# Kernel tuning notes

Measured on AMD Instinct MI355X. Metric: run time of the kernel, lower is better.

## Reference

```python
import jax, jax.numpy as jnp
import numpy as np

H = 8
D_MODEL = 512
D_K = D_MODEL // H
NEG = -1e9


def setup_inputs() -> dict:
    key = jax.random.key(0)
    ks = jax.random.split(key, 12)
    N, Lq, Lk = 2, 4096, 4096
    inp = {
        "query": jax.random.normal(ks[0], (N, Lq, D_MODEL), dtype=jnp.float32),
        "key": jax.random.normal(ks[1], (N, Lk, D_MODEL), dtype=jnp.float32),
        "value": jax.random.normal(ks[2], (N, Lk, D_MODEL), dtype=jnp.float32),
        "mask": jnp.ones((N, 1, Lk), dtype=jnp.int32),
    }
    scale = 0.02
    for i, nm in enumerate(["q", "k", "v", "o"]):
        inp[f"W{nm}"] = scale * jax.random.normal(ks[3 + i], (D_MODEL, D_MODEL), dtype=jnp.float32)
        inp[f"b{nm}"] = jnp.zeros((D_MODEL,), dtype=jnp.float32)
    return inp


def reference(query, key, value, mask, Wq, bq, Wk, bk, Wv, bv, Wo, bo):
    # torch Linear: y = x @ W.T + b
    N, Lq, _ = query.shape
    Lk = key.shape[1]
    q = (query @ Wq.T + bq).reshape(N, Lq, H, D_K)   # (N,Lq,h,dk)
    k = (key @ Wk.T + bk).reshape(N, Lk, H, D_K)     # (N,Lk,h,dk)
    v = (value @ Wv.T + bv).reshape(N, Lk, H, D_K)   # (N,Lk,h,dk)
    # scores: (N,h,Lq,Lk)
    scores = jnp.einsum("bqhd,bkhd->bhqk", q, k) / jnp.sqrt(jnp.float32(D_K))
    # mask (N,1,Lk) or (N,Lq,Lk) -> broadcast over heads (and Lq if singleton)
    m = mask[:, None, :, :]  # (N,1,1|Lq,Lk)
    scores = jnp.where(m == 0, jnp.float32(NEG), scores)
    attn = jax.nn.softmax(scores, axis=-1)
    # dropout is identity in eval mode (deterministic reference)
    out = jnp.einsum("bhqk,bkhd->bqhd", attn, v).reshape(N, Lq, D_MODEL)
    return out @ Wo.T + bo
```

## Files before the change

kernel.cpp:

```cpp
#include <hip/hip_runtime.h>
#include <hip/hip_bf16.h>

#define H 8
#define DM 512
#define DK 64
#define LSEQ 4096
#define NB 2
#define NSPLIT 4
#define KSPAN (LSEQ / NSPLIT)
#define NIT (KSPAN / 64)

#define QSCALE 0.18033688011112042f

typedef float f32x4 __attribute__((ext_vector_type(4)));
typedef __bf16 bf16x8 __attribute__((ext_vector_type(8)));
typedef __bf16 bf16x2 __attribute__((ext_vector_type(2)));
typedef unsigned short u16;

__device__ __forceinline__ u16 f2bf(float f) {
    union { float f; unsigned u; } v{f};
    return (u16)((v.u + 0x8000u) >> 16);
}

__device__ __forceinline__ unsigned pkbf(float a, float b) {
#if __has_builtin(__builtin_amdgcn_cvt_pk_bf16_f32)
    union { bf16x2 v; unsigned u; } x;
    x.v = __builtin_amdgcn_cvt_pk_bf16_f32(a, b);
    return x.u;
#else
    union { float f; unsigned u; } x{a}, y{b};
    return ((x.u + 0x8000u) >> 16) | ((y.u + 0x8000u) & 0xffff0000u);
#endif
}

__device__ __forceinline__ ushort4 cvt4(float4 a) {
    union { ushort4 s; uint2 u; } o;
    o.u.x = pkbf(a.x, a.y);
    o.u.y = pkbf(a.z, a.w);
    return o.s;
}

__device__ __forceinline__ float2 ubf2(unsigned u) {
    union { float f; unsigned v; } a, b;
    a.v = u << 16;
    b.v = u & 0xffff0000u;
    return make_float2(a.f, b.f);
}

__device__ __forceinline__ float fexp2(float x) {
#if __has_builtin(__builtin_amdgcn_exp2f)
    return __builtin_amdgcn_exp2f(x);
#else
    return exp2f(x);
#endif
}

__device__ __forceinline__ f32x4 mfma32(bf16x8 a, bf16x8 b, f32x4 c) {
    return __builtin_amdgcn_mfma_f32_16x16x32_bf16(a, b, c, 0, 0, 0);
}

__launch_bounds__(256, 8)
__global__ void cvt_all(const float* __restrict__ W0, const float* __restrict__ W1,
                        const float* __restrict__ W2, const float* __restrict__ W3,
                        const float* __restrict__ X0, const float* __restrict__ X1,
                        const float* __restrict__ X2,
                        u16* __restrict__ wout, u16* __restrict__ xout)
{
    const int y = blockIdx.y;
    const float* src;
    u16* dst;
    int nblk;
    if (y < 4) {
        src = (y == 0) ? W0 : (y == 1) ? W1 : (y == 2) ? W2 : W3;
        dst = wout + (size_t)y * DM * DM;
        nblk = (DM * DM) / (256 * 8);
    } else {
        src = (y == 4) ? X0 : (y == 5) ? X1 : X2;
        dst = xout + (size_t)(y - 4) * ((size_t)NB * LSEQ * DM);
        nblk = ((size_t)NB * LSEQ * DM) / (256 * 8);
    }
    if ((int)blockIdx.x >= nblk) return;
    size_t base = ((size_t)blockIdx.x * 256 + threadIdx.x) * 8;
    float4 a = *(const float4*)(src + base);
    float4 b = *(const float4*)(src + base + 4);
    *(ushort4*)(dst + base)     = cvt4(a);
    *(ushort4*)(dst + base + 4) = cvt4(b);
}

__launch_bounds__(256, 2)
__global__ void proj_qkv(const u16* __restrict__ xbf,
                         const u16* __restrict__ wbf,
                         const float* __restrict__ bq, const float* __restrict__ bk,
                         const float* __restrict__ bv,
                         const int* __restrict__ mask,
                         u16* __restrict__ qo, u16* __restrict__ ko, u16* __restrict__ vo)
{
    const int mode = blockIdx.z;
    const u16* X      = xbf + (size_t)mode * ((size_t)NB * LSEQ * DM);
    const u16* Wb     = wbf + (size_t)mode * DM * DM;
    const float* bias = (mode == 0) ? bq : (mode == 1) ? bk : bv;
    u16* out          = (mode == 0) ? qo : (mode == 1) ? ko : vo;

    __shared__ __align__(16) u16 As[2][128][72];
    __shared__ __align__(16) u16 Bs[2][128][72];

    const int tid  = threadIdx.x;
    const int wave = tid >> 6;
    const int lane = tid & 63;
    const int g    = lane >> 4;
    const int ln   = lane & 15;
    const int wr   = wave >> 1;
    const int wc   = wave & 1;

    const int m0 = blockIdx.x * 128;
    const int n0 = blockIdx.y * 128;

    uint4 xa[4], wa[4];
    #pragma unroll
    for (int i = 0; i < 4; ++i) {
        int idx = tid + 256 * i;
        int row = idx >> 3;
        int col = (idx & 7) * 8;
        xa[i] = *(const uint4*)(X  + (size_t)(m0 + row) * DM + col);
        wa[i] = *(const uint4*)(Wb + (size_t)(n0 + row) * DM + col);
    }
    #pragma unroll
    for (int i = 0; i < 4; ++i) {
        int idx = tid + 256 * i;
        int row = idx >> 3;
        int col = (idx & 7) * 8;
        *(uint4*)&As[0][row][col] = xa[i];
        *(uint4*)&Bs[0][row][col] = wa[i];
    }

    f32x4 acc[4][4] = {};

    for (int kt = 0; kt < 8; ++kt) {
        const int cur = kt & 1;
        __syncthreads();

        if (kt < 7) {
            int kb = (kt + 1) * 64;
            #pragma unroll
            for (int i = 0; i < 4; ++i) {
                int idx = tid + 256 * i;
                int row = idx >> 3;
                int col = (idx & 7) * 8;
                xa[i] = *(const uint4*)(X  + (size_t)(m0 + row) * DM + kb + col);
                wa[i] = *(const uint4*)(Wb + (size_t)(n0 + row) * DM + kb + col);
            }
        }

        bf16x8 af[4][2], bf[4][2];
        #pragma unroll
        for (int t = 0; t < 4; ++t) {
            af[t][0] = *(const bf16x8*)&As[cur][wr * 64 + t * 16 + ln][g * 8];
            af[t][1] = *(const bf16x8*)&As[cur][wr * 64 + t * 16 + ln][32 + g * 8];
            bf[t][0] = *(const bf16x8*)&Bs[cur][wc * 64 + t * 16 + ln][g * 8];
            bf[t][1] = *(const bf16x8*)&Bs[cur][wc * 64 + t * 16 + ln][32 + g * 8];
        }
        #pragma unroll
        for (int mt = 0; mt < 4; ++mt)
            #pragma unroll
            for (int nt = 0; nt < 4; ++nt) {
                acc[mt][nt] = mfma32(af[mt][0], bf[nt][0], acc[mt][nt]);
                acc[mt][nt] = mfma32(af[mt][1], bf[nt][1], acc[mt][nt]);
            }

        if (kt < 7) {
            int nxt = 1 - cur;
            #pragma unroll
            for (int i = 0; i < 4; ++i) {
                int idx = tid + 256 * i;
                int row = idx >> 3;
                int col = (idx & 7) * 8;
                *(uint4*)&As[nxt][row][col] = xa[i];
                *(uint4*)&Bs[nxt][row][col] = wa[i];
            }
        }
    }

    if (mode != 2) {
        #pragma unroll
        for (int nt = 0; nt < 4; ++nt) {
            int n  = n0 + wc * 64 + nt * 16 + ln;
            float bias_n = bias[n];
            int hh = n >> 6;
            int d  = n & (DK - 1);
            #pragma unroll
            for (int mt = 0; mt < 4; ++mt)
                #pragma unroll
                for (int r = 0; r < 4; ++r) {
                    int m  = m0 + wr * 64 + mt * 16 + g * 4 + r;
                    int bb = m >> 12;
                    int s  = m & (LSEQ - 1);
                    float val = acc[mt][nt][r] + bias_n;
                    if (mode == 0) val *= QSCALE;
                    else           val = mask[bb * LSEQ + s] ? val : 0.0f;
                    out[(size_t)((bb * H + hh) * LSEQ + s) * DK + d] = f2bf(val);
                }
        }
    } else {
        __syncthreads();
        u16* Ts = &As[0][0][0];
        const int bb = m0 >> 12;
        const int s0 = m0 & (LSEQ - 1);
        #pragma unroll
        for (int nt = 0; nt < 4; ++nt) {
            int dl = wc * 64 + nt * 16 + ln;
            float bias_n = bias[n0 + dl];
            #pragma unroll
            for (int mt = 0; mt < 4; ++mt)
                #pragma unroll
                for (int r = 0; r < 4; ++r) {
                    int sl = wr * 64 + mt * 16 + g * 4 + r;
                    float val = acc[mt][nt][r] + bias_n;
                    val = mask[bb * LSEQ + s0 + sl] ? val : 0.0f;
                    Ts[dl * 136 + sl] = f2bf(val);
                }
        }
        __syncthreads();
        int dl   = tid >> 1;
        int half = tid & 1;
        int n  = n0 + dl;
        int hh = n >> 6;
        int d  = n & (DK - 1);
        int sb = s0 + half * 64;
        u16* dst = out + ((size_t)((bb * H + hh) * DK + d) * LSEQ + sb);
        const u16* srcp = Ts + dl * 136 + half * 64;
        #pragma unroll
        for (int i = 0; i < 8; ++i)
            *(uint4*)(dst + i * 8) = *(const uint4*)(srcp + i * 8);
    }
}

__launch_bounds__(256, 4)
__global__ void flash(const u16* __restrict__ qws, const u16* __restrict__ kws,
                      const u16* __restrict__ vws, const int* __restrict__ mask,
                      u16* __restrict__ Opart, float* __restrict__ lpart)
{
    __shared__ u16 Ks[2][64][64];
    __shared__ u16 Vs[2][64][64];

    const int tid   = threadIdx.x;
    const int wave  = tid >> 6;
    const int lane  = tid & 63;
    const int g     = lane >> 4;
    const int ln    = lane & 15;
    const int b     = blockIdx.z;
    const int h     = blockIdx.y;
    const int qblk  = blockIdx.x & 31;
    const int split = blockIdx.x >> 5;
    const int q0    = qblk * 128;
    const int kstart = split * KSPAN;

    const u16* qp = qws + ((size_t)((b * H + h) * LSEQ) + q0 + wave * 32 + ln) * DK;
    const u16* kp = kws + (size_t)(b * H + h) * LSEQ * DK;
    const u16* vp = vws + (size_t)(b * H + h) * DK * LSEQ;
    const int* mp = mask + b * LSEQ;

    int nmask = 0;
    for (int t = 0; t < NIT; ++t) {
        int mval = mp[kstart + t * 64 + lane];
        unsigned long long bal = __ballot(mval == 0);
        nmask += (int)__popcll(bal);
    }
    const float fnmask = (float)nmask;

    bf16x8 qf[2][2];
    qf[0][0] = *(const bf16x8*)(qp + g * 8);
    qf[0][1] = *(const bf16x8*)(qp + 32 + g * 8);
    qf[1][0] = *(const bf16x8*)(qp + 16 * DK + g * 8);
    qf[1][1] = *(const bf16x8*)(qp + 16 * DK + 32 + g * 8);

    union OU { unsigned u[4]; bf16x8 v; } onesu;
    onesu.u[0] = onesu.u[1] = onesu.u[2] = onesu.u[3] = 0x3F803F80u;
    const bf16x8 vones = onesu.v;

    f32x4 accO[2][4] = {};
    f32x4 accL[2] = {};
    const f32x4 fzero = {};

    const int row = tid >> 3;
    const int c   = tid & 7;
    const int swz = row & 7;
    const int kcol = (c ^ swz) * 8;
    const int vcol0 = ((2 * c) & 3) * 16 + (c >> 1) * 4;
    const int vs0 = vcol0 >> 3;
    const int vof = vcol0 & 7;
    const int vw0 = ((vs0 ^ swz) * 8) + vof;
    const int vw1 = (((vs0 + 2) ^ swz) * 8) + vof;
    const int rs = ln & 7;

    uint4 kr0, kr1, vr0, vr1;
    kr0 = *(const uint4*)(kp + (size_t)(kstart + row) * DK + c * 8);
    kr1 = *(const uint4*)(kp + (size_t)(kstart + row + 32) * DK + c * 8);
    vr0 = *(const uint4*)(vp + (size_t)row * LSEQ + kstart + c * 8);
    vr1 = *(const uint4*)(vp + (size_t)(row + 32) * LSEQ + kstart + c * 8);
    *(uint4*)&Ks[0][row][kcol]      = kr0;
    *(uint4*)&Ks[0][row + 32][kcol] = kr1;
    *(uint2*)&Vs[0][row][vw0]       = make_uint2(vr0.x, vr0.y);
    *(uint2*)&Vs[0][row][vw1]       = make_uint2(vr0.z, vr0.w);
    *(uint2*)&Vs[0][row + 32][vw0]  = make_uint2(vr1.x, vr1.y);
    *(uint2*)&Vs[0][row + 32][vw1]  = make_uint2(vr1.z, vr1.w);

    for (int it = 0; it < NIT; ++it) {
        const int cur = it & 1;
        __syncthreads();

        if (it < NIT - 1) {
            int kn = kstart + it * 64 + 64;
            kr0 = *(const uint4*)(kp + (size_t)(kn + row) * DK + c * 8);
            kr1 = *(const uint4*)(kp + (size_t)(kn + row + 32) * DK + c * 8);
            vr0 = *(const uint4*)(vp + (size_t)row * LSEQ + kn + c * 8);
            vr1 = *(const uint4*)(vp + (size_t)(row + 32) * LSEQ + kn + c * 8);
        }

        __builtin_amdgcn_s_setprio(1);
        f32x4 sc[2][4];
        #pragma unroll
        for (int kb = 0; kb < 4; ++kb) {
            bf16x8 kf0 = *(const bf16x8*)&Ks[cur][kb * 16 + ln][(g ^ rs) * 8];
            bf16x8 kf1 = *(const bf16x8*)&Ks[cur][kb * 16 + ln][((g + 4) ^ rs) * 8];
            #pragma unroll
            for (int j = 0; j < 2; ++j) {
                f32x4 z = mfma32(kf0, qf[j][0], fzero);
                z = mfma32(kf1, qf[j][1], z);
                sc[j][kb] = z;
            }
        }
        __builtin_amdgcn_s_setprio(0);

        #pragma unroll
        for (int kb = 0; kb < 4; ++kb)
            #pragma unroll
            for (int j = 0; j < 2; ++j) {
                sc[j][kb][0] = fexp2(sc[j][kb][0]);
                sc[j][kb][1] = fexp2(sc[j][kb][1]);
                sc[j][kb][2] = fexp2(sc[j][kb][2]);
                sc[j][kb][3] = fexp2(sc[j][kb][3]);
            }

        union PU { unsigned u[4]; bf16x8 v; } p01[2], p23[2];
        #pragma unroll
        for (int j = 0; j < 2; ++j) {
            p01[j].u[0] = pkbf(sc[j][0][0], sc[j][0][1]);
            p01[j].u[1] = pkbf(sc[j][0][2], sc[j][0][3]);
            p01[j].u[2] = pkbf(sc[j][1][0], sc[j][1][1]);
            p01[j].u[3] = pkbf(sc[j][1][2], sc[j][1][3]);
            p23[j].u[0] = pkbf(sc[j][2][0], sc[j][2][1]);
            p23[j].u[1] = pkbf(sc[j][2][2], sc[j][2][3]);
            p23[j].u[2] = pkbf(sc[j][3][0], sc[j][3][1]);
            p23[j].u[3] = pkbf(sc[j][3][2], sc[j][3][3]);
        }

        __builtin_amdgcn_s_setprio(1);
        #pragma unroll
        for (int j = 0; j < 2; ++j) {
            accL[j] = mfma32(p01[j].v, vones, accL[j]);
            accL[j] = mfma32(p23[j].v, vones, accL[j]);
        }
        #pragma unroll
        for (int t = 0; t < 4; ++t) {
            bf16x8 vb01 = *(const bf16x8*)&Vs[cur][t * 16 + ln][((2 * g) ^ rs) * 8];
            bf16x8 vb23 = *(const bf16x8*)&Vs[cur][t * 16 + ln][((2 * g + 1) ^ rs) * 8];
            #pragma unroll
            for (int j = 0; j < 2; ++j) {
                accO[j][t] = mfma32(p01[j].v, vb01, accO[j][t]);
                accO[j][t] = mfma32(p23[j].v, vb23, accO[j][t]);
            }
        }
        __builtin_amdgcn_s_setprio(0);

        if (it < NIT - 1) {
            int nxt = 1 - cur;
            *(uint4*)&Ks[nxt][row][kcol]      = kr0;
            *(uint4*)&Ks[nxt][row + 32][kcol] = kr1;
            *(uint2*)&Vs[nxt][row][vw0]       = make_uint2(vr0.x, vr0.y);
            *(uint2*)&Vs[nxt][row][vw1]       = make_uint2(vr0.z, vr0.w);
            *(uint2*)&Vs[nxt][row + 32][vw0]  = make_uint2(vr1.x, vr1.y);
            *(uint2*)&Vs[nxt][row + 32][vw1]  = make_uint2(vr1.z, vr1.w);
        }
    }

    const size_t PLANE = (size_t)NB * LSEQ * DM;
    u16* opp = Opart + (size_t)split * PLANE;

    #pragma unroll
    for (int j = 0; j < 2; ++j) {
        if (ln == 0) {
            #pragma unroll
            for (int r = 0; r < 4; ++r)
                lpart[(size_t)split * (NB * H * LSEQ) + ((size_t)(b * H + h) * LSEQ)
                      + q0 + wave * 32 + j * 16 + g * 4 + r] = accL[j][r] - fnmask;
        }
        #pragma unroll
        for (int r = 0; r < 4; ++r) {
            float linv = 1.0f / (accL[j][r] - fnmask);
            size_t base = ((size_t)(b * LSEQ) + q0 + wave * 32 + j * 16 + g * 4 + r) * DM + h * DK;
            #pragma unroll
            for (int t = 0; t < 4; ++t)
                opp[base + t * 16 + ln] = f2bf(accO[j][t][r] * linv);
        }
    }
}

__launch_bounds__(256, 4)
__global__ void reduce_split(const u16* __restrict__ Opart, const float* __restrict__ lpart,
                             u16* __restrict__ ows)
{
    const size_t PLANE = (size_t)NB * LSEQ * DM;
    const size_t LP    = (size_t)NB * H * LSEQ;
    size_t gid  = (size_t)blockIdx.x * 256 + threadIdx.x;
    size_t flat = gid * 8;

    int b   = (int)(flat >> 21);
    int rem = (int)(flat & ((1 << 21) - 1));
    int q   = rem >> 9;
    int hh  = (rem & 511) >> 6;
    size_t lidx = ((size_t)(b * H + hh) * LSEQ) + q;

    float ls[NSPLIT];
    float lsum = 0.0f;
    #pragma unroll
    for (int s = 0; s < NSPLIT; ++s) {
        ls[s] = lpart[(size_t)s * LP + lidx];
        lsum += ls[s];
    }
    float inv = 1.0f / lsum;

    float o[8] = {};
    #pragma unroll
    for (int s = 0; s < NSPLIT; ++s) {
        float w = ls[s] * inv;
        uint4 cc = *(const uint4*)(Opart + (size_t)s * PLANE + flat);
        float2 a;
        a = ubf2(cc.x); o[0] += w * a.x; o[1] += w * a.y;
        a = ubf2(cc.y); o[2] += w * a.x; o[3] += w * a.y;
        a = ubf2(cc.z); o[4] += w * a.x; o[5] += w * a.y;
        a = ubf2(cc.w); o[6] += w * a.x; o[7] += w * a.y;
    }
    uint4 r;
    r.x = pkbf(o[0], o[1]);
    r.y = pkbf(o[2], o[3]);
    r.z = pkbf(o[4], o[5]);
    r.w = pkbf(o[6], o[7]);
    *(uint4*)(ows + flat) = r;
}

__launch_bounds__(256, 3)
__global__ void proj_out(const u16* __restrict__ A, const u16* __restrict__ Wob,
                         const float* __restrict__ bo, float* __restrict__ out)
{
    __shared__ __align__(16) u16 As[2][128][68];
    __shared__ __align__(16) u16 Bs[2][64][68];

    const int tid  = threadIdx.x;
    const int wave = tid >> 6;
    const int lane = tid & 63;
    const int g    = lane >> 4;
    const int ln   = lane & 15;

    const int m0 = blockIdx.x * 128;
    const int n0 = blockIdx.y * 64;

    uint4 aa[4];
    uint4 wbb[2];
    #pragma unroll
    for (int i = 0; i < 4; ++i) {
        int idx = tid + 256 * i;
        int row = idx >> 3;
        int col = (idx & 7) * 8;
        aa[i] = *(const uint4*)(A + (size_t)(m0 + row) * DM + col);
    }
    #pragma unroll
    for (int i = 0; i < 2; ++i) {
        int idx = tid + 256 * i;
        int rwb = idx >> 3;
        int cwb = (idx & 7) * 8;
        wbb[i] = *(const uint4*)(Wob + (size_t)(n0 + rwb) * DM + cwb);
    }
    #pragma unroll
    for (int i = 0; i < 4; ++i) {
        int idx = tid + 256 * i;
        int row = idx >> 3;
        int col = (idx & 7) * 8;
        *(uint4*)&As[0][row][col] = aa[i];
    }
    #pragma unroll
    for (int i = 0; i < 2; ++i) {
        int idx = tid + 256 * i;
        int rwb = idx >> 3;
        int cwb = (idx & 7) * 8;
        *(uint4*)&Bs[0][rwb][cwb] = wbb[i];
    }

    f32x4 acc[2][4] = {};

    for (int kt = 0; kt < 8; ++kt) {
        const int cur = kt & 1;
        __syncthreads();

        if (kt < 7) {
            int kb = (kt + 1) * 64;
            #pragma unroll
            for (int i = 0; i < 4; ++i) {
                int idx = tid + 256 * i;
                int row = idx >> 3;
                int col = (idx & 7) * 8;
                aa[i] = *(const uint4*)(A + (size_t)(m0 + row) * DM + kb + col);
            }
            #pragma unroll
            for (int i = 0; i < 2; ++i) {
                int idx = tid + 256 * i;
                int rwb = idx >> 3;
                int cwb = (idx & 7) * 8;
                wbb[i] = *(const uint4*)(Wob + (size_t)(n0 + rwb) * DM + kb + cwb);
            }
        }

        bf16x8 af[2][2], bf[4][2];
        #pragma unroll
        for (int mt = 0; mt < 2; ++mt) {
            af[mt][0] = *(const bf16x8*)&As[cur][wave * 32 + mt * 16 + ln][g * 8];
            af[mt][1] = *(const bf16x8*)&As[cur][wave * 32 + mt * 16 + ln][32 + g * 8];
        }
        #pragma unroll
        for (int nt = 0; nt < 4; ++nt) {
            bf[nt][0] = *(const bf16x8*)&Bs[cur][nt * 16 + ln][g * 8];
            bf[nt][1] = *(const bf16x8*)&Bs[cur][nt * 16 + ln][32 + g * 8];
        }
        #pragma unroll
        for (int mt = 0; mt < 2; ++mt)
            #pragma unroll
            for (int nt = 0; nt < 4; ++nt) {
                acc[mt][nt] = mfma32(af[mt][0], bf[nt][0], acc[mt][nt]);
                acc[mt][nt] = mfma32(af[mt][1], bf[nt][1], acc[mt][nt]);
            }

        if (kt < 7) {
            int nxt = 1 - cur;
            #pragma unroll
            for (int i = 0; i < 4; ++i) {
                int idx = tid + 256 * i;
                int row = idx >> 3;
                int col = (idx & 7) * 8;
                *(uint4*)&As[nxt][row][col] = aa[i];
            }
            #pragma unroll
            for (int i = 0; i < 2; ++i) {
                int idx = tid + 256 * i;
                int rwb = idx >> 3;
                int cwb = (idx & 7) * 8;
                *(uint4*)&Bs[nxt][rwb][cwb] = wbb[i];
            }
        }
    }

    #pragma unroll
    for (int nt = 0; nt < 4; ++nt) {
        int n = n0 + nt * 16 + ln;
        float bias_n = bo[n];
        #pragma unroll
        for (int mt = 0; mt < 2; ++mt)
            #pragma unroll
            for (int r = 0; r < 4; ++r) {
                int m = m0 + wave * 32 + mt * 16 + g * 4 + r;
                out[(size_t)m * DM + n] = acc[mt][nt][r] + bias_n;
            }
    }
}

extern "C" void kernel_launch(void* const* d_in, const int* in_sizes, int n_in,
                              void* d_out, int out_size, void* d_ws, size_t ws_size,
                              hipStream_t stream) {
    (void)in_sizes; (void)n_in; (void)out_size; (void)ws_size;

    const float* query = (const float*)d_in[0];
    const float* key   = (const float*)d_in[1];
    const float* value = (const float*)d_in[2];
    const int*   mask  = (const int*)d_in[3];
    const float* Wq = (const float*)d_in[4];
    const float* bq = (const float*)d_in[5];
    const float* Wk = (const float*)d_in[6];
    const float* bk = (const float*)d_in[7];
    const float* Wv = (const float*)d_in[8];
    const float* bv = (const float*)d_in[9];
    const float* Wo = (const float*)d_in[10];
    const float* bo = (const float*)d_in[11];
    float* out = (float*)d_out;

    const size_t PLANE = (size_t)NB * H * LSEQ * DK;
    u16* qws   = (u16*)d_ws;
    u16* kws   = qws + PLANE;
    u16* vws   = kws + PLANE;
    u16* ows   = vws + PLANE;
    u16* Opart = ows + PLANE;
    float* lpart = (float*)(Opart + (size_t)NSPLIT * PLANE);
    u16* wbf   = (u16*)(lpart + (size_t)NSPLIT * NB * H * LSEQ);
    u16* xbf   = Opart;

    dim3 blk(256);
    cvt_all<<<dim3(2048, 7), blk, 0, stream>>>(Wq, Wk, Wv, Wo, query, key, value,
                                               wbf, xbf);
    proj_qkv<<<dim3(64, 4, 3), blk, 0, stream>>>(xbf, wbf, bq, bk, bv, mask,
                                                 qws, kws, vws);
    flash<<<dim3(32 * NSPLIT, H, NB), blk, 0, stream>>>(qws, kws, vws, mask, Opart, lpart);
    reduce_split<<<dim3(2048), blk, 0, stream>>>(Opart, lpart, ows);
    proj_out<<<dim3(64, 8, 1), blk, 0, stream>>>(ows, wbf + 3 * (size_t)DM * DM, bo, out);
}
```

Before: 230.9 us.

## Fuse split-K reduction into flash kernel via last-block atomic counter

Removes the separate reduce_split launch. Each flash block increments a per-(batch, head, q-block) counter, and the last of the NSPLIT blocks to finish combines the partial outputs using the lpart weights and writes ows. The counters are zeroed by an extra grid row added to the conversion kernel. This saves one kernel launch and its pass over global memory, and lets the reduction overlap with flash blocks still running, at the cost of atomics, thread fences and a tail of extra work in some blocks.

```diff
diff --git a/kernel.cpp b/kernel.cpp
--- a/kernel.cpp
+++ b/kernel.cpp
@@ -64,9 +64,17 @@
                         const float* __restrict__ W2, const float* __restrict__ W3,
                         const float* __restrict__ X0, const float* __restrict__ X1,
                         const float* __restrict__ X2,
-                        u16* __restrict__ wout, u16* __restrict__ xout)
+                        u16* __restrict__ wout, u16* __restrict__ xout,
+                        int* __restrict__ cnt)
 {
     const int y = blockIdx.y;
+    if (y == 7) {
+        if (blockIdx.x == 0) {
+            cnt[threadIdx.x] = 0;
+            cnt[threadIdx.x + 256] = 0;
+        }
+        return;
+    }
     const float* src;
     u16* dst;
     int nblk;
@@ -237,7 +245,8 @@
 __launch_bounds__(256, 4)
 __global__ void flash(const u16* __restrict__ qws, const u16* __restrict__ kws,
                       const u16* __restrict__ vws, const int* __restrict__ mask,
-                      u16* __restrict__ Opart, float* __restrict__ lpart)
+                      u16* __restrict__ Opart, float* __restrict__ lpart,
+                      u16* __restrict__ ows, int* __restrict__ cnt)
 {
     __shared__ u16 Ks[2][64][64];
     __shared__ u16 Vs[2][64][64];
@@ -403,49 +412,62 @@
                 opp[base + t * 16 + ln] = f2bf(accO[j][t][r] * linv);
         }
     }
-}
-
-__launch_bounds__(256, 4)
-__global__ void reduce_split(const u16* __restrict__ Opart, const float* __restrict__ lpart,
-                             u16* __restrict__ ows)
-{
-    const size_t PLANE = (size_t)NB * LSEQ * DM;
-    const size_t LP    = (size_t)NB * H * LSEQ;
-    size_t gid  = (size_t)blockIdx.x * 256 + threadIdx.x;
-    size_t flat = gid * 8;
-
-    int b   = (int)(flat >> 21);
-    int rem = (int)(flat & ((1 << 21) - 1));
-    int q   = rem >> 9;
-    int hh  = (rem & 511) >> 6;
-    size_t lidx = ((size_t)(b * H + hh) * LSEQ) + q;
-
-    float ls[NSPLIT];
-    float lsum = 0.0f;
-    #pragma unroll
-    for (int s = 0; s < NSPLIT; ++s) {
-        ls[s] = lpart[(size_t)s * LP + lidx];
-        lsum += ls[s];
-    }
-    float inv = 1.0f / lsum;
-
-    float o[8] = {};
-    #pragma unroll
-    for (int s = 0; s < NSPLIT; ++s) {
-        float w = ls[s] * inv;
-        uint4 cc = *(const uint4*)(Opart + (size_t)s * PLANE + flat);
-        float2 a;
-        a = ubf2(cc.x); o[0] += w * a.x; o[1] += w * a.y;
-        a = ubf2(cc.y); o[2] += w * a.x; o[3] += w * a.y;
-        a = ubf2(cc.z); o[4] += w * a.x; o[5] += w * a.y;
-        a = ubf2(cc.w); o[6] += w * a.x; o[7] += w * a.y;
-    }
-    uint4 r;
-    r.x = pkbf(o[0], o[1]);
-    r.y = pkbf(o[2], o[3]);
-    r.z = pkbf(o[4], o[5]);
-    r.w = pkbf(o[6], o[7]);
-    *(uint4*)(ows + flat) = r;
+
+    volatile int* flg = (volatile int*)&Ks[0][0][0];
+    __syncthreads();
+    if (tid == 0) {
+        __threadfence();
+        int old = atomicAdd(&cnt[(b * H + h) * 32 + qblk], 1);
+        int lastv = (old == NSPLIT - 1) ? 1 : 0;
+        if (lastv) __threadfence();
+        *flg = lastv;
+    }
+    __syncthreads();
+    if (*flg) {
+        const size_t LP = (size_t)NB * H * LSEQ;
+        #pragma unroll
+        for (int p = 0; p < 4; ++p) {
+            int e   = p * 2048 + tid * 8;
+            int qi  = e >> 6;
+            int col = e & 63;
+            size_t lbase = (size_t)(b * H + h) * LSEQ + q0 + qi;
+            float l0 = lpart[lbase];
+            float l1 = lpart[LP + lbase];
+            float l2 = lpart[2 * LP + lbase];
+            float l3 = lpart[3 * LP + lbase];
+            float inv = 1.0f / (l0 + l1 + l2 + l3);
+            float w0 = l0 * inv, w1 = l1 * inv, w2 = l2 * inv, w3 = l3 * inv;
+            size_t fi = ((size_t)(b * LSEQ) + q0 + qi) * DM + h * DK + col;
+            uint4 c0 = *(const uint4*)(Opart + fi);
+            uint4 c1 = *(const uint4*)(Opart + PLANE + fi);
+            uint4 c2 = *(const uint4*)(Opart + 2 * PLANE + fi);
+            uint4 c3 = *(const uint4*)(Opart + 3 * PLANE + fi);
+            float o[8] = {};
+            float2 a;
+            a = ubf2(c0.x); o[0] += w0 * a.x; o[1] += w0 * a.y;
+            a = ubf2(c0.y); o[2] += w0 * a.x; o[3] += w0 * a.y;
+            a = ubf2(c0.z); o[4] += w0 * a.x; o[5] += w0 * a.y;
+            a = ubf2(c0.w); o[6] += w0 * a.x; o[7] += w0 * a.y;
+            a = ubf2(c1.x); o[0] += w1 * a.x; o[1] += w1 * a.y;
+            a = ubf2(c1.y); o[2] += w1 * a.x; o[3] += w1 * a.y;
+            a = ubf2(c1.z); o[4] += w1 * a.x; o[5] += w1 * a.y;
+            a = ubf2(c1.w); o[6] += w1 * a.x; o[7] += w1 * a.y;
+            a = ubf2(c2.x); o[0] += w2 * a.x; o[1] += w2 * a.y;
+            a = ubf2(c2.y); o[2] += w2 * a.x; o[3] += w2 * a.y;
+            a = ubf2(c2.z); o[4] += w2 * a.x; o[5] += w2 * a.y;
+            a = ubf2(c2.w); o[6] += w2 * a.x; o[7] += w2 * a.y;
+            a = ubf2(c3.x); o[0] += w3 * a.x; o[1] += w3 * a.y;
+            a = ubf2(c3.y); o[2] += w3 * a.x; o[3] += w3 * a.y;
+            a = ubf2(c3.z); o[4] += w3 * a.x; o[5] += w3 * a.y;
+            a = ubf2(c3.w); o[6] += w3 * a.x; o[7] += w3 * a.y;
+            uint4 r;
+            r.x = pkbf(o[0], o[1]);
+            r.y = pkbf(o[2], o[3]);
+            r.z = pkbf(o[4], o[5]);
+            r.w = pkbf(o[6], o[7]);
+            *(uint4*)(ows + fi) = r;
+        }
+    }
 }
 
 __launch_bounds__(256, 3)
@@ -598,14 +620,15 @@
     u16* Opart = ows + PLANE;
     float* lpart = (float*)(Opart + (size_t)NSPLIT * PLANE);
     u16* wbf   = (u16*)(lpart + (size_t)NSPLIT * NB * H * LSEQ);
+    int* cnt   = (int*)(wbf + 4 * (size_t)DM * DM);
     u16* xbf   = Opart;
 
     dim3 blk(256);
-    cvt_all<<<dim3(2048, 7), blk, 0, stream>>>(Wq, Wk, Wv, Wo, query, key, value,
-                                               wbf, xbf);
+    cvt_all<<<dim3(2048, 8), blk, 0, stream>>>(Wq, Wk, Wv, Wo, query, key, value,
+                                               wbf, xbf, cnt);
     proj_qkv<<<dim3(64, 4, 3), blk, 0, stream>>>(xbf, wbf, bq, bk, bv, mask,
                                                  qws, kws, vws);
-    flash<<<dim3(32 * NSPLIT, H, NB), blk, 0, stream>>>(qws, kws, vws, mask, Opart, lpart);
-    reduce_split<<<dim3(2048), blk, 0, stream>>>(Opart, lpart, ows);
+    flash<<<dim3(32 * NSPLIT, H, NB), blk, 0, stream>>>(qws, kws, vws, mask,
+                                                        Opart, lpart, ows, cnt);
     proj_out<<<dim3(64, 8, 1), blk, 0, stream>>>(ows, wbf + 3 * (size_t)DM * DM, bo, out);
 }
```

New measurement: 309.6 us. +34.1%, slower.
